# Optimization experiments

Hardware: AMD Instinct MI355X
Metric: run time of the kernel (lower is better)

## Reference

```python
import jax, jax.numpy as jnp
import numpy as np

N_NODES = 50000
N_EDGES = 800000
IN_F = 512
H_F = 32
HEADS = 8
N_CLS = 40
NEG_SLOPE = 0.2


def gat_conv(h, W, al, ar, b, src, dst, n_heads, d_out):
    """DGL-style GATConv. h: [N, F_in]; W: [F_in, n_heads*d_out];
    al, ar: [n_heads, d_out]; b: [n_heads*d_out]. Returns [N, n_heads, d_out]."""
    n = h.shape[0]
    feat = (h @ W).reshape(n, n_heads, d_out)            # [N, H, D]
    el = jnp.sum(feat * al[None], axis=-1)               # [N, H]
    er = jnp.sum(feat * ar[None], axis=-1)               # [N, H]
    e = jax.nn.leaky_relu(el[src] + er[dst], NEG_SLOPE)  # [E, H]
    # numerically stable edge softmax per destination node
    m = jax.ops.segment_max(e, dst, num_segments=n)      # [N, H]
    m = jnp.where(jnp.isfinite(m), m, 0.0)
    ee = jnp.exp(e - m[dst])                             # [E, H]
    den = jax.ops.segment_sum(ee, dst, num_segments=n)   # [N, H]
    alpha = ee / jnp.maximum(den[dst], 1e-9)             # [E, H]
    msg = alpha[:, :, None] * feat[src]                  # [E, H, D]
    rst = jax.ops.segment_sum(msg, dst, num_segments=n)  # [N, H, D]
    return rst + b.reshape(1, n_heads, d_out)


def setup_inputs() -> dict:
    key = jax.random.key(0)
    ks = jax.random.split(key, 16)
    hid = H_F * HEADS
    s = lambda fan: 1.0 / np.sqrt(fan)
    return {
        "in_feat": jax.random.normal(ks[0], (N_NODES, IN_F), jnp.float32),
        "src": jax.random.randint(ks[1], (N_EDGES,), 0, N_NODES, jnp.int32),
        "dst": jax.random.randint(ks[2], (N_EDGES,), 0, N_NODES, jnp.int32),
        "W0": jax.random.normal(ks[3], (IN_F, hid), jnp.float32) * s(IN_F),
        "al0": jax.random.normal(ks[4], (HEADS, H_F), jnp.float32) * s(H_F),
        "ar0": jax.random.normal(ks[5], (HEADS, H_F), jnp.float32) * s(H_F),
        "b0": jnp.zeros((hid,), jnp.float32),
        "W1": jax.random.normal(ks[6], (hid, hid), jnp.float32) * s(hid),
        "al1": jax.random.normal(ks[7], (HEADS, H_F), jnp.float32) * s(H_F),
        "ar1": jax.random.normal(ks[8], (HEADS, H_F), jnp.float32) * s(H_F),
        "b1": jnp.zeros((hid,), jnp.float32),
        "W2": jax.random.normal(ks[9], (hid, N_CLS), jnp.float32) * s(hid),
        "al2": jax.random.normal(ks[10], (1, N_CLS), jnp.float32) * s(N_CLS),
        "ar2": jax.random.normal(ks[11], (1, N_CLS), jnp.float32) * s(N_CLS),
        "b2": jnp.zeros((N_CLS,), jnp.float32),
    }


def reference(in_feat, src, dst, W0, al0, ar0, b0, W1, al1, ar1, b1,
              W2, al2, ar2, b2):
    n = in_feat.shape[0]
    # layer 0 + ReLU (dropout p=0.0 is identity) + flatten heads
    h = gat_conv(in_feat, W0, al0, ar0, b0, src, dst, HEADS, H_F)
    h = jax.nn.relu(h).reshape(n, -1)
    # layer 1
    h = gat_conv(h, W1, al1, ar1, b1, src, dst, HEADS, H_F)
    h = jax.nn.relu(h).reshape(n, -1)
    # output layer, single head, no activation
    h = gat_conv(h, W2, al2, ar2, b2, src, dst, 1, N_CLS)
    return h.reshape(n, -1)
```

## Files before the change

### kernel.cpp

```cpp
#include <hip/hip_runtime.h>
#include <hip/hip_bf16.h>

#define N_NODES 50000
#define N_EDGES 800000
#define IN_F 512
#define HID 256
#define HEADS 8
#define DHEAD 32
#define N_CLS 40
#define NCLS_PAD 64

typedef __bf16 bf16x8 __attribute__((ext_vector_type(8)));
typedef float f32x4 __attribute__((ext_vector_type(4)));

#define AT_AL0 0
#define AT_AR0 256
#define AT_AL1 512
#define AT_AR1 768
#define AT_AL2 1024
#define AT_AR2 1088
#define AT_B0  1152
#define AT_B1  1408
#define AT_B2  1664
#define AT_SZ  1792

__device__ __forceinline__ float ldflag(const void* p, long long i, int isbf) {
  return isbf ? __bfloat162float(((const __hip_bfloat16*)p)[i])
              : ((const float*)p)[i];
}
__device__ __forceinline__ float blo(unsigned u) { return __uint_as_float(u << 16); }
__device__ __forceinline__ float bhi(unsigned u) { return __uint_as_float(u & 0xffff0000u); }
__device__ __forceinline__ unsigned pk2(float a, float b) {
  unsigned x = __bfloat16_as_ushort(__float2bfloat16(a));
  unsigned y = __bfloat16_as_ushort(__float2bfloat16(b));
  return x | (y << 16);
}

__global__ void k_detect_prep(const unsigned short* __restrict__ raw, int* __restrict__ flag,
                              const void* al0, const void* ar0, const void* al1, const void* ar1,
                              const void* al2, const void* ar2, const void* b0, const void* b1,
                              const void* b2, float* __restrict__ att, int* __restrict__ cursor) {
  __shared__ int cnt[256];
  int t = threadIdx.x;
  for (int i = t; i < N_NODES; i += 256) cursor[i] = 0;
  int c = 0;
  for (int i = t; i < 8192; i += 256) {
    int e = (raw[i] >> 7) & 0xFF;
    if (e >= 0x90) c++;
  }
  cnt[t] = c;
  __syncthreads();
  for (int s = 128; s; s >>= 1) {
    if (t < s) cnt[t] += cnt[t + s];
    __syncthreads();
  }
  __shared__ int sflag;
  if (t == 0) { sflag = (cnt[0] > 64) ? 0 : 1; *flag = sflag; }
  __syncthreads();
  int isbf = sflag;
  att[AT_AL0 + t] = ldflag(al0, t, isbf);
  att[AT_AR0 + t] = ldflag(ar0, t, isbf);
  att[AT_AL1 + t] = ldflag(al1, t, isbf);
  att[AT_AR1 + t] = ldflag(ar1, t, isbf);
  att[AT_B0 + t]  = ldflag(b0, t, isbf);
  att[AT_B1 + t]  = ldflag(b1, t, isbf);
  if (t < N_CLS) {
    att[AT_AL2 + t] = ldflag(al2, t, isbf);
    att[AT_AR2 + t] = ldflag(ar2, t, isbf);
    att[AT_B2 + t]  = ldflag(b2, t, isbf);
  }
}

__global__ void k_hist(const int* __restrict__ dst, int* __restrict__ cnt) {
  int e = blockIdx.x * blockDim.x + threadIdx.x;
  if (e < N_EDGES) atomicAdd(&cnt[dst[e]], 1);
}

#define SCAN_B 512
#define SCAN_NB ((N_NODES + SCAN_B - 1) / SCAN_B)

__global__ __launch_bounds__(SCAN_B) void k_scan_blocks(const int* __restrict__ deg,
                                                        int* __restrict__ excl,
                                                        int* __restrict__ partial) {
  __shared__ int buf[SCAN_B];
  int t = threadIdx.x;
  int i = blockIdx.x * SCAN_B + t;
  int v = (i < N_NODES) ? deg[i] : 0;
  buf[t] = v;
  __syncthreads();
  for (int off = 1; off < SCAN_B; off <<= 1) {
    int x = (t >= off) ? buf[t - off] : 0;
    __syncthreads();
    buf[t] += x;
    __syncthreads();
  }
  if (i < N_NODES) excl[i] = buf[t] - v;
  if (t == SCAN_B - 1) partial[blockIdx.x] = buf[t];
}

__global__ void k_scan_partials(int* __restrict__ partial, int* __restrict__ rowptr) {
  __shared__ int buf[SCAN_NB];
  int t = threadIdx.x;
  if (t < SCAN_NB) buf[t] = partial[t];
  __syncthreads();
  if (t == 0) {
    int run = 0;
    for (int b = 0; b < SCAN_NB; b++) { int v = buf[b]; buf[b] = run; run += v; }
    rowptr[N_NODES] = run;
  }
  __syncthreads();
  if (t < SCAN_NB) partial[t] = buf[t];
}

__global__ void k_scan_add(int* __restrict__ rowptr, const int* __restrict__ partial,
                           int* __restrict__ cursor) {
  int i = blockIdx.x * blockDim.x + threadIdx.x;
  if (i < N_NODES) {
    rowptr[i] += partial[i / SCAN_B];
    cursor[i] = 0;
  }
}

__global__ void k_scatter(const int* __restrict__ src, const int* __restrict__ dst,
                          const int* __restrict__ rowptr, int* __restrict__ cursor,
                          int* __restrict__ csr_src) {
  int e = blockIdx.x * blockDim.x + threadIdx.x;
  if (e < N_EDGES) {
    int d = dst[e];
    int pos = rowptr[d] + atomicAdd(&cursor[d], 1);
    csr_src[pos] = src[e];
  }
}

#define TW0 (HID * IN_F)
#define TW1 (TW0 + HID * HID)
#define TW2 (TW1 + NCLS_PAD * HID)
__global__ void k_transpose_all(const void* __restrict__ W0, const void* __restrict__ W1,
                                const void* __restrict__ W2,
                                __hip_bfloat16* __restrict__ w0t, __hip_bfloat16* __restrict__ w1t,
                                __hip_bfloat16* __restrict__ w2t, const int* __restrict__ flag) {
  int isbf = *flag;
  int i = blockIdx.x * blockDim.x + threadIdx.x;
  if (i < TW0) {
    int n = i >> 9, k = i & 511;
    w0t[i] = __float2bfloat16(ldflag(W0, (long long)k * HID + n, isbf));
  } else if (i < TW1) {
    int j = i - TW0;
    int n = j >> 8, k = j & 255;
    w1t[j] = __float2bfloat16(ldflag(W1, (long long)k * HID + n, isbf));
  } else if (i < TW2) {
    int j = i - TW1;
    int n = j >> 8, k = j & 255;
    float v = (n < N_CLS) ? ldflag(W2, (long long)k * N_CLS + n, isbf) : 0.f;
    w2t[j] = __float2bfloat16(v);
  }
}

__device__ __forceinline__ uint4 loadA(const void* A, int isbf, int ga, int M, int K, int off) {
  uint4 av = make_uint4(0u, 0u, 0u, 0u);
  if (ga < M) {
    if (isbf) {
      av = *(const uint4*)((const __hip_bfloat16*)A + (size_t)ga * K + off);
    } else {
      const float* ap = (const float*)A + (size_t)ga * K + off;
      float4 f1 = *(const float4*)ap;
      float4 f2 = *(const float4*)(ap + 4);
      av.x = pk2(f1.x, f1.y); av.y = pk2(f1.z, f1.w);
      av.z = pk2(f2.x, f2.y); av.w = pk2(f2.z, f2.w);
    }
  }
  return av;
}

__global__ __launch_bounds__(256) void k_gemm64(const void* __restrict__ A,
                                                const __hip_bfloat16* __restrict__ Bt,
                                                __hip_bfloat16* __restrict__ C,
                                                int M, int K, int N,
                                                const int* __restrict__ flag, int force_bf,
                                                const float* __restrict__ al,
                                                const float* __restrict__ ar,
                                                float* __restrict__ el,
                                                float* __restrict__ er, int fuse_eler) {
  __shared__ unsigned short As[64][40];
  __shared__ unsigned short Bs[64][40];
  const int isbf = force_bf ? 1 : *flag;
  int nblk = N >> 6;
  int per = nblk << 3;
  int g = blockIdx.x / per;
  int i2 = blockIdx.x - g * per;
  int mb = g * 8 + (i2 & 7);
  int nb = i2 >> 3;
  int m0 = mb * 64, n0 = nb * 64;
  if (m0 >= M) return;
  int tid = threadIdx.x;
  int lrow = tid >> 2;
  int lcol = (tid & 3) * 8;
  int wave = tid >> 6, lane = tid & 63;
  int wm = (wave >> 1) * 32, wn = (wave & 1) * 32;
  int lm = lane & 15, quad = lane >> 4;
  f32x4 acc[2][2] = {};
  uint4 av = loadA(A, isbf, m0 + lrow, M, K, lcol);
  uint4 bv = *(const uint4*)(Bt + (size_t)(n0 + lrow) * K + lcol);
  for (int k0 = 0; k0 < K; k0 += 32) {
    __syncthreads();
    *(uint4*)(&As[lrow][lcol]) = av;
    *(uint4*)(&Bs[lrow][lcol]) = bv;
    __syncthreads();
    uint4 avn = make_uint4(0u, 0u, 0u, 0u), bvn = make_uint4(0u, 0u, 0u, 0u);
    if (k0 + 32 < K) {
      avn = loadA(A, isbf, m0 + lrow, M, K, k0 + 32 + lcol);
      bvn = *(const uint4*)(Bt + (size_t)(n0 + lrow) * K + k0 + 32 + lcol);
    }
    bf16x8 af[2], bfr[2];
    #pragma unroll
    for (int i = 0; i < 2; i++) {
      af[i]  = *(const bf16x8*)(&As[wm + i * 16 + lm][quad * 8]);
      bfr[i] = *(const bf16x8*)(&Bs[wn + i * 16 + lm][quad * 8]);
    }
    #pragma unroll
    for (int mi = 0; mi < 2; mi++)
      #pragma unroll
      for (int ni = 0; ni < 2; ni++)
        acc[mi][ni] = __builtin_amdgcn_mfma_f32_16x16x32_bf16(af[mi], bfr[ni], acc[mi][ni], 0, 0, 0);
    av = avn; bv = bvn;
  }
  #pragma unroll
  for (int mi = 0; mi < 2; mi++)
    #pragma unroll
    for (int ni = 0; ni < 2; ni++)
      #pragma unroll
      for (int r = 0; r < 4; r++) {
        int gm = m0 + wm + mi * 16 + quad * 4 + r;
        int gn = n0 + wn + ni * 16 + lm;
        if (gm < M) C[(size_t)gm * N + gn] = __float2bfloat16(acc[mi][ni][r]);
      }
  if (fuse_eler) {
    int hg = (n0 + wn) >> 5;
    float ala[2], ara[2];
    #pragma unroll
    for (int ni = 0; ni < 2; ni++) {
      ala[ni] = al[hg * DHEAD + ni * 16 + lm];
      ara[ni] = ar[hg * DHEAD + ni * 16 + lm];
    }
    #pragma unroll
    for (int mi = 0; mi < 2; mi++)
      #pragma unroll
      for (int r = 0; r < 4; r++) {
        float pl = acc[mi][0][r] * ala[0] + acc[mi][1][r] * ala[1];
        float pr = acc[mi][0][r] * ara[0] + acc[mi][1][r] * ara[1];
        #pragma unroll
        for (int d = 1; d < 16; d <<= 1) {
          pl += __shfl_xor(pl, d, 16);
          pr += __shfl_xor(pr, d, 16);
        }
        int gm = m0 + wm + mi * 16 + quad * 4 + r;
        if (lm == 0 && gm < M) {
          el[gm * HEADS + hg] = pl;
          er[gm * HEADS + hg] = pr;
        }
      }
  }
}

__global__ void k_eler2(const __hip_bfloat16* __restrict__ feat2,
                        const float* __restrict__ al, const float* __restrict__ ar,
                        float* __restrict__ el, float* __restrict__ er) {
  int n = blockIdx.x * blockDim.x + threadIdx.x;
  if (n >= N_NODES) return;
  const __hip_bfloat16* f = feat2 + (size_t)n * NCLS_PAD;
  float sl = 0.f, sr = 0.f;
  for (int d = 0; d < N_CLS; d++) {
    float v = __bfloat162float(f[d]);
    sl += v * al[d];
    sr += v * ar[d];
  }
  el[n] = sl;
  er[n] = sr;
}

__global__ __launch_bounds__(256) void k_aggregate8(const int* __restrict__ rowptr,
                                                    const int* __restrict__ csr_src,
                                                    const uint4* __restrict__ feat_rows,
                                                    const float* __restrict__ el,
                                                    const float* __restrict__ er,
                                                    const float* __restrict__ bias,
                                                    __hip_bfloat16* __restrict__ out) {
  __shared__ float lds_acc[8][256];
  __shared__ float lds_l[8][32];
  int n = blockIdx.x;
  int t = threadIdx.x;
  int slot = t >> 5;
  int c = t & 31;
  int hh = c >> 2;
  float er_n = er[n * HEADS + hh];
  int beg = rowptr[n], end = rowptr[n + 1];
  float l = 0.f;
  float acc[8] = {0.f, 0.f, 0.f, 0.f, 0.f, 0.f, 0.f, 0.f};
  int i = beg + slot;
  for (; i + 8 < end; i += 16) {
    int s1 = csr_src[i];
    int s2 = csr_src[i + 8];
    float el1 = el[s1 * HEADS + hh];
    float el2 = el[s2 * HEADS + hh];
    uint4 f1 = feat_rows[(size_t)s1 * 32 + c];
    uint4 f2 = feat_rows[(size_t)s2 * 32 + c];
    float x1 = el1 + er_n, x2 = el2 + er_n;
    float e1 = x1 > 0.f ? x1 : 0.2f * x1;
    float e2 = x2 > 0.f ? x2 : 0.2f * x2;
    float p1 = __expf(fminf(e1, 60.f));
    float p2 = __expf(fminf(e2, 60.f));
    l += p1 + p2;
    acc[0] += p1 * blo(f1.x) + p2 * blo(f2.x); acc[1] += p1 * bhi(f1.x) + p2 * bhi(f2.x);
    acc[2] += p1 * blo(f1.y) + p2 * blo(f2.y); acc[3] += p1 * bhi(f1.y) + p2 * bhi(f2.y);
    acc[4] += p1 * blo(f1.z) + p2 * blo(f2.z); acc[5] += p1 * bhi(f1.z) + p2 * bhi(f2.z);
    acc[6] += p1 * blo(f1.w) + p2 * blo(f2.w); acc[7] += p1 * bhi(f1.w) + p2 * bhi(f2.w);
  }
  if (i < end) {
    int s = csr_src[i];
    float elv = el[s * HEADS + hh];
    uint4 fv = feat_rows[(size_t)s * 32 + c];
    float x = elv + er_n;
    float e = x > 0.f ? x : 0.2f * x;
    float p = __expf(fminf(e, 60.f));
    l += p;
    acc[0] += p * blo(fv.x); acc[1] += p * bhi(fv.x);
    acc[2] += p * blo(fv.y); acc[3] += p * bhi(fv.y);
    acc[4] += p * blo(fv.z); acc[5] += p * bhi(fv.z);
    acc[6] += p * blo(fv.w); acc[7] += p * bhi(fv.w);
  }
  *(float4*)&lds_acc[slot][c * 8]     = make_float4(acc[0], acc[1], acc[2], acc[3]);
  *(float4*)&lds_acc[slot][c * 8 + 4] = make_float4(acc[4], acc[5], acc[6], acc[7]);
  lds_l[slot][c] = l;
  __syncthreads();
  float a = 0.f, L = 0.f;
  #pragma unroll
  for (int s2 = 0; s2 < 8; s2++) { a += lds_acc[s2][t]; L += lds_l[s2][t >> 3]; }
  float o = a / fmaxf(L, 1e-9f) + bias[t];
  o = fmaxf(o, 0.f);
  out[(size_t)n * HID + t] = __float2bfloat16(o);
}

__global__ __launch_bounds__(256) void k_aggregate1(const int* __restrict__ rowptr,
                                                    const int* __restrict__ csr_src,
                                                    const uint4* __restrict__ fr2,
                                                    const float* __restrict__ el,
                                                    const float* __restrict__ er,
                                                    const float* __restrict__ bias,
                                                    void* __restrict__ out,
                                                    const int* __restrict__ flag) {
  __shared__ float lds_acc[32][64];
  __shared__ float lds_l[32][8];
  int isbf = *flag;
  int n = blockIdx.x;
  int t = threadIdx.x;
  int slot = t >> 3;
  int c = t & 7;
  float er_n = er[n];
  int beg = rowptr[n], end = rowptr[n + 1];
  float l = 0.f;
  float acc[8] = {0.f, 0.f, 0.f, 0.f, 0.f, 0.f, 0.f, 0.f};
  int i = beg + slot;
  for (; i + 32 < end; i += 64) {
    int s1 = csr_src[i], s2 = csr_src[i + 32];
    float el1 = el[s1], el2 = el[s2];
    uint4 f1 = fr2[(size_t)s1 * 8 + c];
    uint4 f2 = fr2[(size_t)s2 * 8 + c];
    float x1 = el1 + er_n, x2 = el2 + er_n;
    float e1 = x1 > 0.f ? x1 : 0.2f * x1;
    float e2 = x2 > 0.f ? x2 : 0.2f * x2;
    float p1 = __expf(fminf(e1, 60.f));
    float p2 = __expf(fminf(e2, 60.f));
    l += p1 + p2;
    acc[0] += p1 * blo(f1.x) + p2 * blo(f2.x); acc[1] += p1 * bhi(f1.x) + p2 * bhi(f2.x);
    acc[2] += p1 * blo(f1.y) + p2 * blo(f2.y); acc[3] += p1 * bhi(f1.y) + p2 * bhi(f2.y);
    acc[4] += p1 * blo(f1.z) + p2 * blo(f2.z); acc[5] += p1 * bhi(f1.z) + p2 * bhi(f2.z);
    acc[6] += p1 * blo(f1.w) + p2 * blo(f2.w); acc[7] += p1 * bhi(f1.w) + p2 * bhi(f2.w);
  }
  if (i < end) {
    int s = csr_src[i];
    float x = el[s] + er_n;
    uint4 fv = fr2[(size_t)s * 8 + c];
    float e = x > 0.f ? x : 0.2f * x;
    float p = __expf(fminf(e, 60.f));
    l += p;
    acc[0] += p * blo(fv.x); acc[1] += p * bhi(fv.x);
    acc[2] += p * blo(fv.y); acc[3] += p * bhi(fv.y);
    acc[4] += p * blo(fv.z); acc[5] += p * bhi(fv.z);
    acc[6] += p * blo(fv.w); acc[7] += p * bhi(fv.w);
  }
  *(float4*)&lds_acc[slot][c * 8]     = make_float4(acc[0], acc[1], acc[2], acc[3]);
  *(float4*)&lds_acc[slot][c * 8 + 4] = make_float4(acc[4], acc[5], acc[6], acc[7]);
  lds_l[slot][c] = l;
  __syncthreads();
  if (t < N_CLS) {
    float a = 0.f, L = 0.f;
    #pragma unroll
    for (int s2 = 0; s2 < 32; s2++) { a += lds_acc[s2][t]; L += lds_l[s2][t >> 3]; }
    float o = a / fmaxf(L, 1e-9f) + bias[t];
    if (isbf) ((__hip_bfloat16*)out)[(size_t)n * N_CLS + t] = __float2bfloat16(o);
    else      ((float*)out)[(size_t)n * N_CLS + t] = o;
  }
}

static inline size_t align_up(size_t x) { return (x + 255) & ~(size_t)255; }

extern "C" void kernel_launch(void* const* d_in, const int* in_sizes, int n_in,
                              void* d_out, int out_size, void* d_ws, size_t ws_size,
                              hipStream_t stream) {
  const void* in_feat = d_in[0];
  const int* src = (const int*)d_in[1];
  const int* dst = (const int*)d_in[2];
  const void* W0  = d_in[3];
  const void* al0 = d_in[4];
  const void* ar0 = d_in[5];
  const void* b0  = d_in[6];
  const void* W1  = d_in[7];
  const void* al1 = d_in[8];
  const void* ar1 = d_in[9];
  const void* b1  = d_in[10];
  const void* W2  = d_in[11];
  const void* al2 = d_in[12];
  const void* ar2 = d_in[13];
  const void* b2  = d_in[14];

  char* p = (char*)d_ws;
  int* flag = (int*)p;                   p += 256;
  float* att = (float*)p;                p += align_up(AT_SZ * sizeof(float));
  int* rowptr = (int*)p;                 p += align_up((N_NODES + 1) * sizeof(int));
  int* cursor = (int*)p;                 p += align_up(N_NODES * sizeof(int));
  int* csr_src = (int*)p;                p += align_up(N_EDGES * sizeof(int));
  int* partial = (int*)p;                p += align_up(SCAN_NB * sizeof(int));
  __hip_bfloat16* feat16 = (__hip_bfloat16*)p; p += align_up((size_t)N_NODES * HID * sizeof(__hip_bfloat16));
  __hip_bfloat16* h16 = (__hip_bfloat16*)p;    p += align_up((size_t)N_NODES * HID * sizeof(__hip_bfloat16));
  float* el = (float*)p;                 p += align_up((size_t)N_NODES * HEADS * sizeof(float));
  float* er = (float*)p;                 p += align_up((size_t)N_NODES * HEADS * sizeof(float));
  __hip_bfloat16* w0t = (__hip_bfloat16*)p;    p += align_up((size_t)HID * IN_F * sizeof(__hip_bfloat16));
  __hip_bfloat16* w1t = (__hip_bfloat16*)p;    p += align_up((size_t)HID * HID * sizeof(__hip_bfloat16));
  __hip_bfloat16* w2t = (__hip_bfloat16*)p;    p += align_up((size_t)NCLS_PAD * HID * sizeof(__hip_bfloat16));

  const int EB = (N_EDGES + 255) / 256;
  const int MB64 = (N_NODES + 63) / 64;
  const int GROUPS = (MB64 + 7) / 8;
  const int G4 = GROUPS * 8 * 4;
  const int G1 = GROUPS * 8 * 1;

  k_detect_prep<<<1, 256, 0, stream>>>((const unsigned short*)in_feat, flag,
                                       al0, ar0, al1, ar1, al2, ar2, b0, b1, b2, att, cursor);

  k_hist<<<EB, 256, 0, stream>>>(dst, cursor);
  k_scan_blocks<<<SCAN_NB, SCAN_B, 0, stream>>>(cursor, rowptr, partial);
  k_scan_partials<<<1, 128, 0, stream>>>(partial, rowptr);
  k_scan_add<<<(N_NODES + 255) / 256, 256, 0, stream>>>(rowptr, partial, cursor);
  k_scatter<<<EB, 256, 0, stream>>>(src, dst, rowptr, cursor, csr_src);

  k_transpose_all<<<(TW2 + 255) / 256, 256, 0, stream>>>(W0, W1, W2, w0t, w1t, w2t, flag);

  k_gemm64<<<G4, 256, 0, stream>>>(in_feat, w0t, feat16, N_NODES, IN_F, HID, flag, 0,
                                   att + AT_AL0, att + AT_AR0, el, er, 1);
  k_aggregate8<<<N_NODES, 256, 0, stream>>>(rowptr, csr_src, (const uint4*)feat16, el, er, att + AT_B0, h16);

  k_gemm64<<<G4, 256, 0, stream>>>(h16, w1t, feat16, N_NODES, HID, HID, flag, 1,
                                   att + AT_AL1, att + AT_AR1, el, er, 1);
  k_aggregate8<<<N_NODES, 256, 0, stream>>>(rowptr, csr_src, (const uint4*)feat16, el, er, att + AT_B1, h16);

  k_gemm64<<<G1, 256, 0, stream>>>(h16, w2t, feat16, N_NODES, HID, NCLS_PAD, flag, 1,
                                   nullptr, nullptr, nullptr, nullptr, 0);
  k_eler2<<<(N_NODES + 255) / 256, 256, 0, stream>>>(feat16, att + AT_AL2, att + AT_AR2, el, er);
  k_aggregate1<<<N_NODES, 256, 0, stream>>>(rowptr, csr_src, (const uint4*)feat16, el, er, att + AT_B2, d_out, flag);
}
```

Before: 531.9 us.

## Add 128x128-tile MFMA GEMM with direct global-to-LDS loads for hidden layers

Adds a new GEMM kernel that uses 128x128 output tiles with a 128-deep K phase. Loads go straight into XOR-swizzled LDS via global_load_lds, and block indices are remapped across the XCDs. It replaces the 64-wide tile GEMM for the two 256-wide hidden-layer projections and keeps the fused el/er computation. The larger tiles mean more reuse per loaded element and fewer blocks. The cost is 64 KB of LDS per block, which limits occupancy, and there is no double-buffering, so loads and compute do not overlap.

```diff
diff --git a/kernel.cpp b/kernel.cpp
--- a/kernel.cpp
+++ b/kernel.cpp
@@ -34,6 +34,10 @@
   unsigned x = __bfloat16_as_ushort(__float2bfloat16(a));
   unsigned y = __bfloat16_as_ushort(__float2bfloat16(b));
   return x | (y << 16);
+}
+__device__ __forceinline__ void gload16(const unsigned short* g, unsigned short* l) {
+  __builtin_amdgcn_global_load_lds((__attribute__((address_space(1))) void*)g,
+                                   (__attribute__((address_space(3))) void*)l, 16, 0, 0);
 }
 
 __global__ void k_detect_prep(const unsigned short* __restrict__ raw, int* __restrict__ flag,
@@ -170,6 +174,131 @@
     }
   }
   return av;
+}
+
+__global__ __launch_bounds__(256) void k_gemm128b(const void* __restrict__ A,
+                                                  const __hip_bfloat16* __restrict__ Bt,
+                                                  __hip_bfloat16* __restrict__ C,
+                                                  int M, int K, int N,
+                                                  const int* __restrict__ flag, int force_bf,
+                                                  const float* __restrict__ al,
+                                                  const float* __restrict__ ar,
+                                                  float* __restrict__ el,
+                                                  float* __restrict__ er, int fuse_eler) {
+  __shared__ unsigned short sA[128 * 128];
+  __shared__ unsigned short sB[128 * 128];
+  const int isbf = force_bf ? 1 : *flag;
+  int nwg = gridDim.x;
+  int q = nwg >> 3, r = nwg & 7;
+  int xcd = blockIdx.x & 7, lid = blockIdx.x >> 3;
+  int logical = (xcd < r ? xcd * (q + 1) : r * (q + 1) + (xcd - r) * q) + lid;
+  int nblk = N >> 7;
+  int mb = logical / nblk;
+  int nb = logical - mb * nblk;
+  int m0 = mb << 7, n0 = nb << 7;
+  int tid = threadIdx.x;
+  int lane = tid & 63, wave = tid >> 6;
+  int wm = (wave >> 1) << 6, wn = (wave & 1) << 6;
+  int lm = lane & 15, quad = lane >> 4;
+  int rbase = tid >> 4;
+  int srcoff = ((tid & 15) ^ rbase) << 3;
+  const unsigned short* Ab = (const unsigned short*)A;
+  const float* Af = (const float*)A;
+  const unsigned short* Bb = (const unsigned short*)Bt;
+  size_t abase[8];
+  size_t bbase[8];
+  #pragma unroll
+  for (int i = 0; i < 8; i++) {
+    int row = (i << 4) + rbase;
+    int ga = m0 + row; if (ga > M - 1) ga = M - 1;
+    abase[i] = (size_t)ga * K + srcoff;
+    bbase[i] = (size_t)(n0 + row) * K + srcoff;
+  }
+  f32x4 acc[4][4] = {};
+  int nph = K >> 7;
+  for (int ph = 0; ph < nph; ++ph) {
+    int kph = ph << 7;
+    if (isbf) {
+      #pragma unroll
+      for (int i = 0; i < 8; i++) {
+        gload16(Ab + abase[i] + kph, &sA[(((i << 8) + tid) << 3)]);
+        gload16(Bb + bbase[i] + kph, &sB[(((i << 8) + tid) << 3)]);
+      }
+    } else {
+      #pragma unroll
+      for (int i = 0; i < 8; i++) {
+        gload16(Bb + bbase[i] + kph, &sB[(((i << 8) + tid) << 3)]);
+        const float* p0 = Af + abase[i] + kph;
+        float4 x = *(const float4*)p0;
+        float4 y = *(const float4*)(p0 + 4);
+        *(uint4*)&sA[(((i << 8) + tid) << 3)] =
+            make_uint4(pk2(x.x, x.y), pk2(x.z, x.w), pk2(y.x, y.y), pk2(y.z, y.w));
+      }
+    }
+    __syncthreads();
+    #pragma unroll
+    for (int s = 0; s < 4; s++) {
+      bf16x8 af[4], bfr[4];
+      #pragma unroll
+      for (int i = 0; i < 4; i++) {
+        int ra = wm + (i << 4) + lm;
+        int rb = wn + (i << 4) + lm;
+        int sl = (((s << 2) + quad) ^ lm) << 3;
+        af[i]  = *(const bf16x8*)&sA[(ra << 7) + sl];
+        bfr[i] = *(const bf16x8*)&sB[(rb << 7) + sl];
+      }
+      #pragma unroll
+      for (int mi = 0; mi < 4; mi++)
+        #pragma unroll
+        for (int ni = 0; ni < 4; ni++)
+          acc[mi][ni] = __builtin_amdgcn_mfma_f32_16x16x32_bf16(af[mi], bfr[ni], acc[mi][ni], 0, 0, 0);
+    }
+    __syncthreads();
+  }
+  #pragma unroll
+  for (int mi = 0; mi < 4; mi++) {
+    #pragma unroll
+    for (int r2 = 0; r2 < 4; r2++) {
+      int gm = m0 + wm + mi * 16 + (quad << 2) + r2;
+      if (gm < M) {
+        #pragma unroll
+        for (int ni = 0; ni < 4; ni++) {
+          int gn = n0 + wn + ni * 16 + lm;
+          C[(size_t)gm * N + gn] = __float2bfloat16(acc[mi][ni][r2]);
+        }
+      }
+    }
+  }
+  if (fuse_eler) {
+    int h0 = (n0 + wn) >> 5;
+    float ala[4], ara[4];
+    #pragma unroll
+    for (int ni = 0; ni < 4; ni++) {
+      int idx = (h0 + (ni >> 1)) * DHEAD + ((ni & 1) << 4) + lm;
+      ala[ni] = al[idx];
+      ara[ni] = ar[idx];
+    }
+    #pragma unroll
+    for (int mi = 0; mi < 4; mi++)
+      #pragma unroll
+      for (int r2 = 0; r2 < 4; r2++) {
+        int gm = m0 + wm + mi * 16 + (quad << 2) + r2;
+        #pragma unroll
+        for (int hp = 0; hp < 2; hp++) {
+          float pl = acc[mi][2 * hp][r2] * ala[2 * hp] + acc[mi][2 * hp + 1][r2] * ala[2 * hp + 1];
+          float pr = acc[mi][2 * hp][r2] * ara[2 * hp] + acc[mi][2 * hp + 1][r2] * ara[2 * hp + 1];
+          #pragma unroll
+          for (int d = 1; d < 16; d <<= 1) {
+            pl += __shfl_xor(pl, d, 16);
+            pr += __shfl_xor(pr, d, 16);
+          }
+          if (lm == 0 && gm < M) {
+            el[gm * HEADS + h0 + hp] = pl;
+            er[gm * HEADS + h0 + hp] = pr;
+          }
+        }
+      }
+  }
 }
 
 __global__ __launch_bounds__(256) void k_gemm64(const void* __restrict__ A,
@@ -441,8 +570,9 @@
   const int EB = (N_EDGES + 255) / 256;
   const int MB64 = (N_NODES + 63) / 64;
   const int GROUPS = (MB64 + 7) / 8;
-  const int G4 = GROUPS * 8 * 4;
   const int G1 = GROUPS * 8 * 1;
+  const int MB128 = (N_NODES + 127) / 128;
+  const int GX = MB128 * 2;
 
   k_detect_prep<<<1, 256, 0, stream>>>((const unsigned short*)in_feat, flag,
                                        al0, ar0, al1, ar1, al2, ar2, b0, b1, b2, att, cursor);
@@ -455,12 +585,12 @@
 
   k_transpose_all<<<(TW2 + 255) / 256, 256, 0, stream>>>(W0, W1, W2, w0t, w1t, w2t, flag);
 
-  k_gemm64<<<G4, 256, 0, stream>>>(in_feat, w0t, feat16, N_NODES, IN_F, HID, flag, 0,
-                                   att + AT_AL0, att + AT_AR0, el, er, 1);
+  k_gemm128b<<<GX, 256, 0, stream>>>(in_feat, w0t, feat16, N_NODES, IN_F, HID, flag, 0,
+                                     att + AT_AL0, att + AT_AR0, el, er, 1);
   k_aggregate8<<<N_NODES, 256, 0, stream>>>(rowptr, csr_src, (const uint4*)feat16, el, er, att + AT_B0, h16);
 
-  k_gemm64<<<G4, 256, 0, stream>>>(h16, w1t, feat16, N_NODES, HID, HID, flag, 1,
-                                   att + AT_AL1, att + AT_AR1, el, er, 1);
+  k_gemm128b<<<GX, 256, 0, stream>>>(h16, w1t, feat16, N_NODES, HID, HID, flag, 1,
+                                     att + AT_AL1, att + AT_AR1, el, er, 1);
   k_aggregate8<<<N_NODES, 256, 0, stream>>>(rowptr, csr_src, (const uint4*)feat16, el, er, att + AT_B1, h16);
 
   k_gemm64<<<G1, 256, 0, stream>>>(h16, w2t, feat16, N_NODES, HID, NCLS_PAD, flag, 1,
```

Result: no change. 533.1 us (+0.2%).
